# Kernel optimization log

Measured on AMD Instinct MI355X. Metric: run time of the kernel, lower is better.

Reference implementation:

```python
import jax, jax.numpy as jnp
import numpy as np

CUTOFFS = [0, 20000, 40000, 50000]
B, S, D = 2, 1024, 256

def setup_inputs() -> dict:
    key = jax.random.key(0)
    ks = jax.random.split(key, 6)
    x = jax.random.normal(ks[0], (B, S, D), dtype=jnp.float32)
    targets = jax.random.randint(ks[1], (B, S), 0, CUTOFFS[-1], dtype=jnp.int64)
    scale = 1.0 / np.sqrt(D)
    w0 = jax.random.normal(ks[2], (CUTOFFS[1] - CUTOFFS[0], D), dtype=jnp.float32) * scale
    w1 = jax.random.normal(ks[3], (CUTOFFS[2] - CUTOFFS[1], D), dtype=jnp.float32) * scale
    w2 = jax.random.normal(ks[4], (CUTOFFS[3] - CUTOFFS[2], D), dtype=jnp.float32) * scale
    b0 = jnp.zeros((CUTOFFS[1] - CUTOFFS[0],), dtype=jnp.float32)
    b1 = jnp.zeros((CUTOFFS[2] - CUTOFFS[1],), dtype=jnp.float32)
    b2 = jnp.zeros((CUTOFFS[3] - CUTOFFS[2],), dtype=jnp.float32)
    return {"x": x, "targets": targets, "w0": w0, "w1": w1, "w2": w2,
            "b0": b0, "b1": b1, "b2": b2}

def reference(x, targets, w0, w1, w2, b0, b1, b2):
    # Faithful to TF: for each cluster, compute dense logits for ALL tokens,
    # zero out positions whose target id is outside [l, r) (scatter_nd of the
    # boolean-masked logits into a zeros tensor == multiply by mask), concat
    # along vocab, then log_softmax over the full vocab.
    ws = [w0, w1, w2]
    bs = [b0, b1, b2]
    pieces = []
    for i in range(len(CUTOFFS) - 1):
        l, r = CUTOFFS[i], CUTOFFS[i + 1]
        mask = ((targets >= l) & (targets < r)).astype(x.dtype)[..., None]  # [B,S,1]
        logits = jnp.einsum('bsd,vd->bsv', x, ws[i]) + bs[i]               # [B,S,r-l]
        pieces.append(logits * mask)
    out = jnp.concatenate(pieces, axis=-1)  # [B,S,n_token]
    return jax.nn.log_softmax(out, axis=-1)
```

## Files before the change

### kernel.cpp

```cpp
#include <hip/hip_runtime.h>
#include <hip/hip_bf16.h>
#include <math.h>


typedef __attribute__((ext_vector_type(4))) float f32x4;
typedef __attribute__((ext_vector_type(8))) short bf16x8;
typedef __attribute__((ext_vector_type(4))) unsigned short u16x4;
typedef __attribute__((ext_vector_type(8))) unsigned short u16x8;

__device__ __forceinline__ unsigned int f2bf(float f) {
    union { float f; unsigned int u; } cv; cv.f = f;
    unsigned int u = cv.u + 0x7fffu + ((cv.u >> 16) & 1u);
    return u >> 16;
}
__device__ __forceinline__ float bf2f(unsigned short h) {
    union { unsigned int u; float f; } cv; cv.u = ((unsigned int)h) << 16;
    return cv.f;
}

__global__ __launch_bounds__(1024) void classify_kernel(
    const int* __restrict__ targets, int* cnt, int* lists,
    int n_tok, int c1, int c2) {
    __shared__ int lcnt[3];
    int tid = threadIdx.x;
    if (tid < 3) lcnt[tid] = 0;
    __syncthreads();
    for (int t = tid; t < n_tok; t += 1024) {
        int tgt = targets[t];
        int c = (tgt < c1) ? 0 : ((tgt < c2) ? 1 : 2);
        int pos = atomicAdd(&lcnt[c], 1);
        lists[c * n_tok + pos] = t;
    }
    __syncthreads();
    if (tid < 3) cnt[tid] = lcnt[tid];
}

__global__ __launch_bounds__(512) void pack_a_kernel(
    const float* __restrict__ x, const int* __restrict__ lists,
    const int* __restrict__ cnt, unsigned short* __restrict__ packA,
    int n_tok) {
    int it0 = (cnt[0] + 255) >> 8, it1 = (cnt[1] + 255) >> 8,
        it2 = (cnt[2] + 255) >> 8;
    int g0 = it0 * 16, g1 = it1 * 16, g2 = it2 * 16;
    int gb = blockIdx.x;
    int c, g, n, base;
    if (gb < g0)                { c = 0; g = gb;            n = cnt[0]; base = 0; }
    else if (gb < g0 + g1)      { c = 1; g = gb - g0;       n = cnt[1]; base = g0; }
    else if (gb < g0 + g1 + g2) { c = 2; g = gb - g0 - g1;  n = cnt[2]; base = g0 + g1; }
    else return;

    int tid = threadIdx.x;
    int k0 = tid >> 6, lane = tid & 63;
    int l15 = lane & 15, lg = lane >> 4;
    int pos = g * 16 + l15;
    int tok = (pos < n) ? lists[c * n_tok + pos] : -1;
    uint4 pk = make_uint4(0u, 0u, 0u, 0u);
    if (tok >= 0) {
        const float* src = x + (size_t)tok * 256 + k0 * 32 + lg * 8;
        float4 lo = *(const float4*)src;
        float4 hi = *(const float4*)(src + 4);
        pk.x = f2bf(lo.x) | (f2bf(lo.y) << 16);
        pk.y = f2bf(lo.z) | (f2bf(lo.w) << 16);
        pk.z = f2bf(hi.x) | (f2bf(hi.y) << 16);
        pk.w = f2bf(hi.z) | (f2bf(hi.w) << 16);
    }
    *(uint4*)(packA + ((size_t)(base + g) * 8 + k0) * 512 + lane * 8) = pk;
}

__global__ __launch_bounds__(256, 3) void gemm_ws_kernel(
    const unsigned short* __restrict__ packA,
    const float* __restrict__ w0, const float* __restrict__ w1,
    const float* __restrict__ w2,
    const float* __restrict__ b0, const float* __restrict__ b1,
    const float* __restrict__ b2,
    const int* __restrict__ lists, const int* __restrict__ cnt,
    int V0, int V1, int V2, int nv0, int nv1,
    unsigned short* __restrict__ lws, int lstride, int n_tok) {

    __shared__ __align__(16) unsigned char wlds[64 * 512];
    __shared__ int tok_lds[2048];

    int bid = blockIdx.x;
    int c, vt;
    if (bid < nv0)            { c = 0; vt = bid; }
    else if (bid < nv0 + nv1) { c = 1; vt = bid - nv0; }
    else                      { c = 2; vt = bid - nv0 - nv1; }

    const float* Wc; const float* Bc; int Vc;
    if (c == 0)      { Wc = w0; Bc = b0; Vc = V0; }
    else if (c == 1) { Wc = w1; Bc = b1; Vc = V1; }
    else             { Wc = w2; Bc = b2; Vc = V2; }

    int it0 = (cnt[0] + 255) >> 8, it1 = (cnt[1] + 255) >> 8;
    int baseg = (c == 0) ? 0 : ((c == 1) ? it0 * 16 : (it0 + it1) * 16);

    int n = cnt[c];
    int nIter = (n + 255) >> 8;
    int v0 = vt * 64;
    int tid = threadIdx.x;

    #pragma unroll
    for (int u0 = 0; u0 < 2; ++u0) {
        int u = u0 * 256 + tid;
        int row = u >> 3, seg = u & 7;
        int v = v0 + row;
        float4 f[8];
        if (v < Vc) {
            const float* src = Wc + (size_t)v * 256 + seg * 32;
            #pragma unroll
            for (int j = 0; j < 8; ++j) f[j] = *(const float4*)(src + j * 4);
        } else {
            #pragma unroll
            for (int j = 0; j < 8; ++j) f[j] = make_float4(0.f, 0.f, 0.f, 0.f);
        }
        unsigned fb = (unsigned)(((row >> 4) * 8 + seg) * 1024);
        int l15r = row & 15;
        #pragma unroll
        for (int j = 0; j < 4; ++j) {
            uint4 pk;
            pk.x = f2bf(f[2*j].x)   | (f2bf(f[2*j].y)   << 16);
            pk.y = f2bf(f[2*j].z)   | (f2bf(f[2*j].w)   << 16);
            pk.z = f2bf(f[2*j+1].x) | (f2bf(f[2*j+1].y) << 16);
            pk.w = f2bf(f[2*j+1].z) | (f2bf(f[2*j+1].w) << 16);
            *(uint4*)(wlds + fb + (j * 16 + l15r) * 16) = pk;
        }
    }
    for (int i = tid; i < nIter * 256; i += 256)
        tok_lds[i] = (i < n) ? lists[c * n_tok + i] : -1;
    __syncthreads();

    int lane = tid & 63;
    int wid  = tid >> 6;
    int lg = lane >> 4, l15 = lane & 15;
    const char* pA = (const char*)packA;

    float bvv[4][4];
    #pragma unroll
    for (int mv = 0; mv < 4; ++mv) {
        int vbase = v0 + mv * 16 + lg * 4;
        #pragma unroll
        for (int r = 0; r < 4; ++r)
            bvv[mv][r] = (vbase + r < Vc) ? Bc[vbase + r]
                                          : -__builtin_huge_valf();
    }

    for (int it = 0; it < nIter; ++it) {
        int tb = it * 256 + wid * 64;
        if (tb >= n) continue;
        const char* ga = pA + (size_t)(baseg + it * 16 + wid * 4) * 8192 + lane * 16;

        f32x4 acc[4][4];
        #pragma unroll
        for (int mv = 0; mv < 4; ++mv)
            #pragma unroll
            for (int nt = 0; nt < 4; ++nt)
                acc[mv][nt] = (f32x4){0.f, 0.f, 0.f, 0.f};

        #pragma unroll
        for (int k0 = 0; k0 < 8; ++k0) {
            bf16x8 w[4], xf[4];
            #pragma unroll
            for (int mv = 0; mv < 4; ++mv)
                w[mv] = *(const bf16x8*)(wlds + (mv * 8 + k0) * 1024 + lane * 16);
            #pragma unroll
            for (int nt = 0; nt < 4; ++nt)
                xf[nt] = *(const bf16x8*)(ga + nt * 8192 + k0 * 1024);
            #pragma unroll
            for (int mv = 0; mv < 4; ++mv)
                #pragma unroll
                for (int nt = 0; nt < 4; ++nt)
                    acc[mv][nt] = __builtin_amdgcn_mfma_f32_16x16x32_bf16(
                        w[mv], xf[nt], acc[mv][nt], 0, 0, 0);
        }

        #pragma unroll
        for (int nt = 0; nt < 4; ++nt) {
            int tokid = tok_lds[tb + nt * 16 + l15];
            if (tokid >= 0) {
                unsigned short* dst =
                    lws + (size_t)tokid * lstride + v0 + lg * 4;
                #pragma unroll
                for (int mv = 0; mv < 4; ++mv) {
                    u16x4 pk;
                    pk.x = (unsigned short)f2bf(acc[mv][nt][0] + bvv[mv][0]);
                    pk.y = (unsigned short)f2bf(acc[mv][nt][1] + bvv[mv][1]);
                    pk.z = (unsigned short)f2bf(acc[mv][nt][2] + bvv[mv][2]);
                    pk.w = (unsigned short)f2bf(acc[mv][nt][3] + bvv[mv][3]);
                    *(u16x4*)(dst + mv * 16) = pk;
                }
            }
        }
    }
}

__global__ __launch_bounds__(256) void finalize_kernel(
    float* __restrict__ out, const unsigned short* __restrict__ lws,
    int lstride, const int* __restrict__ targets, int c1, int c2, int N) {
    __shared__ float sred[4];
    __shared__ float sL;

    int t = blockIdx.x;
    int tid = threadIdx.x;
    int tgt = targets[t];
    int l, r, V;
    if (tgt < c1)      { l = 0;  r = c1; V = c1; }
    else if (tgt < c2) { l = c1; r = c2; V = c2 - c1; }
    else               { l = c2; r = N;  V = N - c2; }

    const unsigned short* lrow = lws + (size_t)t * lstride;
    int Vp8 = (V + 7) & ~7;

    float s = 0.f;
    for (int i = tid * 8; i < Vp8; i += 2048) {
        u16x8 u = *(const u16x8*)(lrow + i);
        s += __expf(bf2f(u.s0)) + __expf(bf2f(u.s1))
           + __expf(bf2f(u.s2)) + __expf(bf2f(u.s3))
           + __expf(bf2f(u.s4)) + __expf(bf2f(u.s5))
           + __expf(bf2f(u.s6)) + __expf(bf2f(u.s7));
    }
    s += __shfl_down(s, 32); s += __shfl_down(s, 16); s += __shfl_down(s, 8);
    s += __shfl_down(s, 4);  s += __shfl_down(s, 2);  s += __shfl_down(s, 1);
    if ((tid & 63) == 0) sred[tid >> 6] = s;
    __syncthreads();
    if (tid == 0)
        sL = logf(sred[0] + sred[1] + sred[2] + sred[3] + (float)(N - V));
    __syncthreads();
    float L = sL;

    float* orow = out + (size_t)t * N;
    f32x4 neg = (f32x4){-L, -L, -L, -L};
    for (int i4 = tid * 4; i4 < N; i4 += 1024) {
        f32x4 res;
        if (i4 >= l && i4 < r) {
            u16x4 u = *(const u16x4*)(lrow + (i4 - l));
            res = (f32x4){bf2f(u.x) - L, bf2f(u.y) - L,
                          bf2f(u.z) - L, bf2f(u.w) - L};
        } else {
            res = neg;
        }
        __builtin_nontemporal_store(res, (f32x4*)(orow + i4));
    }
}

extern "C" void kernel_launch(void* const* d_in, const int* in_sizes, int n_in,
                              void* d_out, int out_size, void* d_ws, size_t ws_size,
                              hipStream_t stream) {
    const float* x       = (const float*)d_in[0];
    const int*   targets = (const int*)d_in[1];
    const float* w0      = (const float*)d_in[2];
    const float* w1      = (const float*)d_in[3];
    const float* w2      = (const float*)d_in[4];
    const float* b0      = (const float*)d_in[5];
    const float* b1      = (const float*)d_in[6];
    const float* b2      = (const float*)d_in[7];
    float* out = (float*)d_out;

    int n_tok = in_sizes[1];
    int V0 = in_sizes[5];
    int V1 = in_sizes[6];
    int V2 = in_sizes[7];
    int N  = V0 + V1 + V2;
    int c1 = V0, c2 = V0 + V1;
    int nv0 = (V0 + 63) >> 6, nv1 = (V1 + 63) >> 6, nv2 = (V2 + 63) >> 6;
    int maxV = V0 > V1 ? V0 : V1; if (V2 > maxV) maxV = V2;
    int lstride = ((maxV + 63) >> 6) << 6;

    int maxGroups = (((n_tok + 255) >> 8) + 3) << 4;

    char* ws = (char*)d_ws;
    size_t off = 0;
    int* cnt = (int*)(ws + off);      off += 256;
    int* lists = (int*)(ws + off);    off += (((size_t)3 * n_tok * 4 + 255) & ~(size_t)255);
    unsigned short* packA = (unsigned short*)(ws + off);
    off += (((size_t)maxGroups * 8192 + 255) & ~(size_t)255);
    unsigned short* lws = (unsigned short*)(ws + off);

    classify_kernel<<<1, 1024, 0, stream>>>(targets, cnt, lists, n_tok, c1, c2);

    pack_a_kernel<<<maxGroups, 512, 0, stream>>>(x, lists, cnt, packA, n_tok);

    gemm_ws_kernel<<<nv0 + nv1 + nv2, 256, 0, stream>>>(
        packA, w0, w1, w2, b0, b1, b2, lists, cnt,
        V0, V1, V2, nv0, nv1, lws, lstride, n_tok);

    finalize_kernel<<<n_tok, 256, 0, stream>>>(
        out, lws, lstride, targets, c1, c2, N);
}
```

Measured before the change: 151.5 us.

## Stage GEMM epilogue through LDS and cache logit rows in finalize registers

```diff
diff --git a/kernel.cpp b/kernel.cpp
--- a/kernel.cpp
+++ b/kernel.cpp
@@ -67,6 +67,7 @@
     *(uint4*)(packA + ((size_t)(base + g) * 8 + k0) * 512 + lane * 8) = pk;
 }
 
+#define TROW 136
 __global__ __launch_bounds__(256, 3) void gemm_ws_kernel(
     const unsigned short* __restrict__ packA,
     const float* __restrict__ w0, const float* __restrict__ w1,
@@ -79,6 +80,7 @@
 
     __shared__ __align__(16) unsigned char wlds[64 * 512];
     __shared__ int tok_lds[2048];
+    __shared__ __align__(16) unsigned char tlds[4 * 16 * TROW];
 
     int bid = blockIdx.x;
     int c, vt;
@@ -133,6 +135,7 @@
     int wid  = tid >> 6;
     int lg = lane >> 4, l15 = lane & 15;
     const char* pA = (const char*)packA;
+    unsigned char* tb = tlds + wid * (16 * TROW);
 
     float bvv[4][4];
     #pragma unroll
@@ -143,10 +146,11 @@
             bvv[mv][r] = (vbase + r < Vc) ? Bc[vbase + r]
                                           : -__builtin_huge_valf();
     }
+    int t16 = lane >> 2, prt = lane & 3;
 
     for (int it = 0; it < nIter; ++it) {
-        int tb = it * 256 + wid * 64;
-        if (tb >= n) continue;
+        int tbase = it * 256 + wid * 64;
+        if (tbase >= n) continue;
         const char* ga = pA + (size_t)(baseg + it * 16 + wid * 4) * 8192 + lane * 16;
 
         f32x4 acc[4][4];
@@ -175,25 +179,37 @@
 
         #pragma unroll
         for (int nt = 0; nt < 4; ++nt) {
-            int tokid = tok_lds[tb + nt * 16 + l15];
+            #pragma unroll
+            for (int mv = 0; mv < 4; ++mv) {
+                u16x4 pk;
+                pk.x = (unsigned short)f2bf(acc[mv][nt][0] + bvv[mv][0]);
+                pk.y = (unsigned short)f2bf(acc[mv][nt][1] + bvv[mv][1]);
+                pk.z = (unsigned short)f2bf(acc[mv][nt][2] + bvv[mv][2]);
+                pk.w = (unsigned short)f2bf(acc[mv][nt][3] + bvv[mv][3]);
+                *(u16x4*)(tb + l15 * TROW + mv * 32 + lg * 8) = pk;
+            }
+            asm volatile("s_waitcnt lgkmcnt(0)" ::: "memory");
+            __builtin_amdgcn_sched_barrier(0);
+            const unsigned char* rb = tb + t16 * TROW + prt * 16;
+            u16x4 a0 = *(const u16x4*)(rb + 0);
+            u16x4 a1 = *(const u16x4*)(rb + 8);
+            u16x4 b0v = *(const u16x4*)(rb + 64);
+            u16x4 b1v = *(const u16x4*)(rb + 72);
+            int tokid = tok_lds[tbase + nt * 16 + t16];
             if (tokid >= 0) {
-                unsigned short* dst =
-                    lws + (size_t)tokid * lstride + v0 + lg * 4;
-                #pragma unroll
-                for (int mv = 0; mv < 4; ++mv) {
-                    u16x4 pk;
-                    pk.x = (unsigned short)f2bf(acc[mv][nt][0] + bvv[mv][0]);
-                    pk.y = (unsigned short)f2bf(acc[mv][nt][1] + bvv[mv][1]);
-                    pk.z = (unsigned short)f2bf(acc[mv][nt][2] + bvv[mv][2]);
-                    pk.w = (unsigned short)f2bf(acc[mv][nt][3] + bvv[mv][3]);
-                    *(u16x4*)(dst + mv * 16) = pk;
-                }
-            }
-        }
-    }
-}
-
-__global__ __launch_bounds__(256) void finalize_kernel(
+                unsigned short* dst = lws + (size_t)tokid * lstride + v0 + prt * 8;
+                u16x8 s0 = {a0.x, a0.y, a0.z, a0.w, a1.x, a1.y, a1.z, a1.w};
+                u16x8 s1 = {b0v.x, b0v.y, b0v.z, b0v.w, b1v.x, b1v.y, b1v.z, b1v.w};
+                *(u16x8*)dst = s0;
+                *(u16x8*)(dst + 32) = s1;
+            }
+            asm volatile("s_waitcnt lgkmcnt(0)" ::: "memory");
+            __builtin_amdgcn_sched_barrier(0);
+        }
+    }
+}
+
+__global__ __launch_bounds__(256, 4) void finalize_kernel(
     float* __restrict__ out, const unsigned short* __restrict__ lws,
     int lstride, const int* __restrict__ targets, int c1, int c2, int N) {
     __shared__ float sred[4];
@@ -209,14 +225,31 @@
 
     const unsigned short* lrow = lws + (size_t)t * lstride;
     int Vp8 = (V + 7) & ~7;
-
+    bool cached = (Vp8 <= 20480);
+
+    u16x8 rc[10];
     float s = 0.f;
-    for (int i = tid * 8; i < Vp8; i += 2048) {
-        u16x8 u = *(const u16x8*)(lrow + i);
-        s += __expf(bf2f(u.s0)) + __expf(bf2f(u.s1))
-           + __expf(bf2f(u.s2)) + __expf(bf2f(u.s3))
-           + __expf(bf2f(u.s4)) + __expf(bf2f(u.s5))
-           + __expf(bf2f(u.s6)) + __expf(bf2f(u.s7));
+    if (cached) {
+        #pragma unroll
+        for (int j = 0; j < 10; ++j) {
+            int idx = tid * 8 + j * 2048;
+            if (idx < Vp8) {
+                u16x8 u = *(const u16x8*)(lrow + idx);
+                rc[j] = u;
+                s += __expf(bf2f(u.s0)) + __expf(bf2f(u.s1))
+                   + __expf(bf2f(u.s2)) + __expf(bf2f(u.s3))
+                   + __expf(bf2f(u.s4)) + __expf(bf2f(u.s5))
+                   + __expf(bf2f(u.s6)) + __expf(bf2f(u.s7));
+            }
+        }
+    } else {
+        for (int i = tid * 8; i < Vp8; i += 2048) {
+            u16x8 u = *(const u16x8*)(lrow + i);
+            s += __expf(bf2f(u.s0)) + __expf(bf2f(u.s1))
+               + __expf(bf2f(u.s2)) + __expf(bf2f(u.s3))
+               + __expf(bf2f(u.s4)) + __expf(bf2f(u.s5))
+               + __expf(bf2f(u.s6)) + __expf(bf2f(u.s7));
+        }
     }
     s += __shfl_down(s, 32); s += __shfl_down(s, 16); s += __shfl_down(s, 8);
     s += __shfl_down(s, 4);  s += __shfl_down(s, 2);  s += __shfl_down(s, 1);
@@ -228,18 +261,54 @@
     float L = sL;
 
     float* orow = out + (size_t)t * N;
+    if (cached) {
+        #pragma unroll
+        for (int j = 0; j < 10; ++j) {
+            int idx = tid * 8 + j * 2048;
+            if (idx < Vp8) {
+                u16x8 u = rc[j];
+                if (idx + 8 <= V) {
+                    f32x4 r0 = (f32x4){bf2f(u.s0) - L, bf2f(u.s1) - L,
+                                       bf2f(u.s2) - L, bf2f(u.s3) - L};
+                    f32x4 r1 = (f32x4){bf2f(u.s4) - L, bf2f(u.s5) - L,
+                                       bf2f(u.s6) - L, bf2f(u.s7) - L};
+                    __builtin_nontemporal_store(r0, (f32x4*)(orow + l + idx));
+                    __builtin_nontemporal_store(r1, (f32x4*)(orow + l + idx + 4));
+                } else {
+                    float vals[8] = {bf2f(u.s0), bf2f(u.s1), bf2f(u.s2),
+                                     bf2f(u.s3), bf2f(u.s4), bf2f(u.s5),
+                                     bf2f(u.s6), bf2f(u.s7)};
+                    #pragma unroll
+                    for (int k = 0; k < 8; ++k)
+                        if (idx + k < V) orow[l + idx + k] = vals[k] - L;
+                }
+            }
+        }
+    } else {
+        for (int i = tid * 8; i < Vp8; i += 2048) {
+            u16x8 u = *(const u16x8*)(lrow + i);
+            if (i + 8 <= V) {
+                f32x4 r0 = (f32x4){bf2f(u.s0) - L, bf2f(u.s1) - L,
+                                   bf2f(u.s2) - L, bf2f(u.s3) - L};
+                f32x4 r1 = (f32x4){bf2f(u.s4) - L, bf2f(u.s5) - L,
+                                   bf2f(u.s6) - L, bf2f(u.s7) - L};
+                __builtin_nontemporal_store(r0, (f32x4*)(orow + l + i));
+                __builtin_nontemporal_store(r1, (f32x4*)(orow + l + i + 4));
+            } else {
+                float vals[8] = {bf2f(u.s0), bf2f(u.s1), bf2f(u.s2),
+                                 bf2f(u.s3), bf2f(u.s4), bf2f(u.s5),
+                                 bf2f(u.s6), bf2f(u.s7)};
+                #pragma unroll
+                for (int k = 0; k < 8; ++k)
+                    if (i + k < V) orow[l + i + k] = vals[k] - L;
+            }
+        }
+    }
     f32x4 neg = (f32x4){-L, -L, -L, -L};
-    for (int i4 = tid * 4; i4 < N; i4 += 1024) {
-        f32x4 res;
-        if (i4 >= l && i4 < r) {
-            u16x4 u = *(const u16x4*)(lrow + (i4 - l));
-            res = (f32x4){bf2f(u.x) - L, bf2f(u.y) - L,
-                          bf2f(u.z) - L, bf2f(u.w) - L};
-        } else {
-            res = neg;
-        }
-        __builtin_nontemporal_store(res, (f32x4*)(orow + i4));
-    }
+    for (int i4 = tid * 4; i4 < l; i4 += 1024)
+        __builtin_nontemporal_store(neg, (f32x4*)(orow + i4));
+    for (int i4 = r + tid * 4; i4 < N; i4 += 1024)
+        __builtin_nontemporal_store(neg, (f32x4*)(orow + i4));
 }
 
 extern "C" void kernel_launch(void* const* d_in, const int* in_sizes, int n_in,
```

Measured after the change: 170.9 us. 12.8% more time.

## Fuse exp-sum into GEMM epilogue and add per-token log-sum-exp reduce kernel

Applied to the files above, without the earlier changes.

```diff
diff --git a/kernel.cpp b/kernel.cpp
--- a/kernel.cpp
+++ b/kernel.cpp
@@ -6,7 +6,6 @@
 typedef __attribute__((ext_vector_type(4))) float f32x4;
 typedef __attribute__((ext_vector_type(8))) short bf16x8;
 typedef __attribute__((ext_vector_type(4))) unsigned short u16x4;
-typedef __attribute__((ext_vector_type(8))) unsigned short u16x8;
 
 __device__ __forceinline__ unsigned int f2bf(float f) {
     union { float f; unsigned int u; } cv; cv.f = f;
@@ -75,7 +74,8 @@
     const float* __restrict__ b2,
     const int* __restrict__ lists, const int* __restrict__ cnt,
     int V0, int V1, int V2, int nv0, int nv1,
-    unsigned short* __restrict__ lws, int lstride, int n_tok) {
+    unsigned short* __restrict__ lws, int lstride,
+    float* __restrict__ psum, int n_tok) {
 
     __shared__ __align__(16) unsigned char wlds[64 * 512];
     __shared__ int tok_lds[2048];
@@ -176,57 +176,63 @@
         #pragma unroll
         for (int nt = 0; nt < 4; ++nt) {
             int tokid = tok_lds[tb + nt * 16 + l15];
-            if (tokid >= 0) {
-                unsigned short* dst =
-                    lws + (size_t)tokid * lstride + v0 + lg * 4;
-                #pragma unroll
-                for (int mv = 0; mv < 4; ++mv) {
+            float se = 0.f;
+            unsigned short* dst =
+                lws + (size_t)(tokid < 0 ? 0 : tokid) * lstride + v0 + lg * 4;
+            #pragma unroll
+            for (int mv = 0; mv < 4; ++mv) {
+                float g0 = acc[mv][nt][0] + bvv[mv][0];
+                float g1 = acc[mv][nt][1] + bvv[mv][1];
+                float g2 = acc[mv][nt][2] + bvv[mv][2];
+                float g3 = acc[mv][nt][3] + bvv[mv][3];
+                se += __expf(g0) + __expf(g1) + __expf(g2) + __expf(g3);
+                if (tokid >= 0) {
                     u16x4 pk;
-                    pk.x = (unsigned short)f2bf(acc[mv][nt][0] + bvv[mv][0]);
-                    pk.y = (unsigned short)f2bf(acc[mv][nt][1] + bvv[mv][1]);
-                    pk.z = (unsigned short)f2bf(acc[mv][nt][2] + bvv[mv][2]);
-                    pk.w = (unsigned short)f2bf(acc[mv][nt][3] + bvv[mv][3]);
+                    pk.x = (unsigned short)f2bf(g0);
+                    pk.y = (unsigned short)f2bf(g1);
+                    pk.z = (unsigned short)f2bf(g2);
+                    pk.w = (unsigned short)f2bf(g3);
                     *(u16x4*)(dst + mv * 16) = pk;
                 }
             }
-        }
-    }
+            se += __shfl_xor(se, 16);
+            se += __shfl_xor(se, 32);
+            if (tokid >= 0 && lg == 0)
+                psum[(size_t)vt * n_tok + tokid] = se;
+        }
+    }
+}
+
+__global__ __launch_bounds__(256) void lse_reduce_kernel(
+    const float* __restrict__ psum, const int* __restrict__ targets,
+    float* __restrict__ lse, int c1, int c2, int N, int n_tok) {
+    int t = blockIdx.x * 256 + threadIdx.x;
+    if (t >= n_tok) return;
+    int tgt = targets[t];
+    int V;
+    if (tgt < c1)      V = c1;
+    else if (tgt < c2) V = c2 - c1;
+    else               V = N - c2;
+    int nv = (V + 63) >> 6;
+    float s = 0.f;
+    for (int i = 0; i < nv; ++i) s += psum[(size_t)i * n_tok + t];
+    lse[t] = logf(s + (float)(N - V));
 }
 
 __global__ __launch_bounds__(256) void finalize_kernel(
     float* __restrict__ out, const unsigned short* __restrict__ lws,
-    int lstride, const int* __restrict__ targets, int c1, int c2, int N) {
-    __shared__ float sred[4];
-    __shared__ float sL;
-
+    int lstride, const int* __restrict__ targets,
+    const float* __restrict__ lse, int c1, int c2, int N) {
     int t = blockIdx.x;
     int tid = threadIdx.x;
     int tgt = targets[t];
-    int l, r, V;
-    if (tgt < c1)      { l = 0;  r = c1; V = c1; }
-    else if (tgt < c2) { l = c1; r = c2; V = c2 - c1; }
-    else               { l = c2; r = N;  V = N - c2; }
+    int l, r;
+    if (tgt < c1)      { l = 0;  r = c1; }
+    else if (tgt < c2) { l = c1; r = c2; }
+    else               { l = c2; r = N;  }
+    float L = lse[t];
 
     const unsigned short* lrow = lws + (size_t)t * lstride;
-    int Vp8 = (V + 7) & ~7;
-
-    float s = 0.f;
-    for (int i = tid * 8; i < Vp8; i += 2048) {
-        u16x8 u = *(const u16x8*)(lrow + i);
-        s += __expf(bf2f(u.s0)) + __expf(bf2f(u.s1))
-           + __expf(bf2f(u.s2)) + __expf(bf2f(u.s3))
-           + __expf(bf2f(u.s4)) + __expf(bf2f(u.s5))
-           + __expf(bf2f(u.s6)) + __expf(bf2f(u.s7));
-    }
-    s += __shfl_down(s, 32); s += __shfl_down(s, 16); s += __shfl_down(s, 8);
-    s += __shfl_down(s, 4);  s += __shfl_down(s, 2);  s += __shfl_down(s, 1);
-    if ((tid & 63) == 0) sred[tid >> 6] = s;
-    __syncthreads();
-    if (tid == 0)
-        sL = logf(sred[0] + sred[1] + sred[2] + sred[3] + (float)(N - V));
-    __syncthreads();
-    float L = sL;
-
     float* orow = out + (size_t)t * N;
     f32x4 neg = (f32x4){-L, -L, -L, -L};
     for (int i4 = tid * 4; i4 < N; i4 += 1024) {
@@ -264,6 +270,7 @@
     int nv0 = (V0 + 63) >> 6, nv1 = (V1 + 63) >> 6, nv2 = (V2 + 63) >> 6;
     int maxV = V0 > V1 ? V0 : V1; if (V2 > maxV) maxV = V2;
     int lstride = ((maxV + 63) >> 6) << 6;
+    int maxNv = (maxV + 63) >> 6;
 
     int maxGroups = (((n_tok + 255) >> 8) + 3) << 4;
 
@@ -271,6 +278,8 @@
     size_t off = 0;
     int* cnt = (int*)(ws + off);      off += 256;
     int* lists = (int*)(ws + off);    off += (((size_t)3 * n_tok * 4 + 255) & ~(size_t)255);
+    float* psum = (float*)(ws + off); off += (((size_t)maxNv * n_tok * 4 + 255) & ~(size_t)255);
+    float* lse = (float*)(ws + off);  off += (((size_t)n_tok * 4 + 255) & ~(size_t)255);
     unsigned short* packA = (unsigned short*)(ws + off);
     off += (((size_t)maxGroups * 8192 + 255) & ~(size_t)255);
     unsigned short* lws = (unsigned short*)(ws + off);
@@ -281,8 +290,11 @@
 
     gemm_ws_kernel<<<nv0 + nv1 + nv2, 256, 0, stream>>>(
         packA, w0, w1, w2, b0, b1, b2, lists, cnt,
-        V0, V1, V2, nv0, nv1, lws, lstride, n_tok);
+        V0, V1, V2, nv0, nv1, lws, lstride, psum, n_tok);
+
+    lse_reduce_kernel<<<(n_tok + 255) / 256, 256, 0, stream>>>(
+        psum, targets, lse, c1, c2, N, n_tok);
 
     finalize_kernel<<<n_tok, 256, 0, stream>>>(
-        out, lws, lstride, targets, c1, c2, N);
-}
+        out, lws, lstride, targets, lse, c1, c2, N);
+}
```

New measurement: 219.9 us. 45.2% more time.
